# Kernel tuning notes

Hardware: AMD Instinct MI355X
Metric: run time of the kernel (lower is better)

The kernel has to match this reference:

```python
import jax, jax.numpy as jnp
import numpy as np
from jax import lax

HIDDEN = 256      # hidden_dim
LATENT = 128      # latent_dim
VOCAB = 32000     # vocab_size
MAX_LEN = 64      # max_len (stack capacity guard, as in original)
MAX_STEPS = 128   # fixed step budget for the decode stack machine
N_NODES = 511     # complete binary tree, depth 9


def _linear_params(key, fan_in, fan_out):
    k1, k2 = jax.random.split(key)
    s = 1.0 / np.sqrt(fan_in)
    W = jax.random.uniform(k1, (fan_out, fan_in), minval=-s, maxval=s, dtype=jnp.float32)
    b = jax.random.uniform(k2, (fan_out,), minval=-s, maxval=s, dtype=jnp.float32)
    return W, b


def setup_inputs() -> dict:
    key = jax.random.key(0)
    ks = jax.random.split(key, 10)
    embed = jax.random.normal(ks[0], (VOCAB, HIDDEN), dtype=jnp.float32)
    Wpar, bpar = _linear_params(ks[1], 3 * HIDDEN, HIDDEN)
    Wmu, bmu = _linear_params(ks[2], HIDDEN, LATENT)
    Wlv, blv = _linear_params(ks[3], HIDDEN, LATENT)
    W1, b1 = _linear_params(ks[4], LATENT, HIDDEN)
    W2, b2 = _linear_params(ks[5], HIDDEN, HIDDEN + 1)
    Wl, bl = _linear_params(ks[6], HIDDEN, VOCAB)
    Wp, bp = _linear_params(ks[7], HIDDEN, 2 * LATENT + VOCAB)
    values = jax.random.randint(ks[8], (N_NODES,), 0, VOCAB)
    idx = np.arange(N_NODES)
    left = np.where(2 * idx + 1 < N_NODES, 2 * idx + 1, -1).astype(np.int32)
    right = np.where(2 * idx + 2 < N_NODES, 2 * idx + 2, -1).astype(np.int32)
    eps = jax.random.normal(ks[9], (LATENT,), dtype=jnp.float32)
    return dict(embed=embed, Wpar=Wpar, bpar=bpar, Wmu=Wmu, bmu=bmu,
                Wlv=Wlv, blv=blv, W1=W1, b1=b1, W2=W2, b2=b2,
                Wl=Wl, bl=bl, Wp=Wp, bp=bp, eps=eps,
                values=jnp.asarray(values), left=jnp.asarray(left), right=jnp.asarray(right))


def reference(embed, Wpar, bpar, Wmu, bmu, Wlv, blv, W1, b1, W2, b2,
              Wl, bl, Wp, bp, eps, values, left, right):
    # ---------- encode: bottom-up over tree stored as index arrays ----------
    emb = embed[values]  # [N, H], one gather for all node embeddings

    def enc_step(h, i):
        v = emb[i]
        li = jnp.maximum(left[i], 0)
        ri = jnp.maximum(right[i], 0)
        cat = jnp.concatenate([v, h[li], h[ri]])          # [3H]
        hp = cat @ Wpar.T + bpar                           # parent combine
        hi = jnp.where(left[i] < 0, v, hp)                 # leaf -> embedding
        return h.at[i].set(hi), None

    h0 = jnp.zeros((values.shape[0], HIDDEN), dtype=embed.dtype)
    # children have larger index than parents -> process in descending order
    h, _ = lax.scan(enc_step, h0, jnp.arange(values.shape[0] - 1, -1, -1))
    root = h[0]
    mu = root @ Wmu.T + bmu
    logvar = root @ Wlv.T + blv
    z = mu + eps * jnp.exp(0.5 * logvar)                   # reparameterize

    # ---------- decode: stack machine with fixed step budget ----------
    V, L = VOCAB, LATENT
    stack0 = jnp.zeros((MAX_LEN, L), dtype=z.dtype).at[0].set(z)
    out0 = jnp.zeros((MAX_STEPS, V), dtype=z.dtype)

    def dec_step(state, _):
        stack, sp, out, op = state
        active = sp > 0
        idx = jnp.maximum(sp - 1, 0)
        node = stack[idx]                                  # pop
        hmid = jax.nn.leaky_relu(node @ W1.T + b1, 0.2)
        co = hmid @ W2.T + b2                              # [H+1]; co[0] = gate
        is_parent = (co[0] > 0) & (sp - 1 <= MAX_LEN - 2) & active

        def parent_fn(_):
            dec = co[1:] @ Wp.T + bp                       # [V + 2L]
            value = dec[:V]
            ll = dec[V:V + L]
            rl = dec[V + L:]
            # original appends llatent then rlatent -> rlatent on top
            st = stack.at[idx].set(ll).at[idx + 1].set(rl)
            return value, st, sp + 1

        def leaf_fn(_):
            return co[1:] @ Wl.T + bl, stack, sp - 1

        value, st, nsp = lax.cond(is_parent, parent_fn, leaf_fn, None)
        m = active.astype(z.dtype)
        out = out.at[op].add(m * value)                    # rows written once
        stack = jnp.where(active, st, stack)
        sp = jnp.where(active, nsp, sp)
        op = op + active.astype(op.dtype)
        return (stack, sp, out, op), None

    init = (stack0, jnp.int32(1), out0, jnp.int32(0))
    (_, _, out, _), _ = lax.scan(dec_step, init, None, length=MAX_STEPS)
    return out, mu, logvar
```

## Files before the change

kernel.cpp:

```cpp
#include <hip/hip_runtime.h>

#define HID 256
#define LAT 128
#define VOC 32000
#define NSTEP 128

__global__ __launch_bounds__(512)
void prep_kernel(const float* __restrict__ Wp, const float* __restrict__ W2,
                 const float* __restrict__ b2, const float* __restrict__ bp,
                 const float* __restrict__ Wpar,
                 const float* __restrict__ Wmu, const float* __restrict__ Wlv,
                 float* __restrict__ Wcomb, float* __restrict__ bcomb,
                 float* __restrict__ Wq_par, float* __restrict__ Wq_mu,
                 float* __restrict__ Wq_lv, float* __restrict__ Wq_w2) {
    const int b = blockIdx.x;
    const int t = threadIdx.x;
    if (b < 256) {
        const int o = b;
        const int k = t & 255, jh = t >> 8;
        __shared__ float wpt_s[256];
        __shared__ float part_s[2][256];
        __shared__ float red_s[4];
        if (t < 256) wpt_s[t] = Wp[(size_t)(VOC + o) * HID + t];
        __syncthreads();
        float acc = 0.f;
#pragma unroll 8
        for (int j = 0; j < 128; j++)
            acc += wpt_s[jh * 128 + j] * W2[(size_t)(1 + jh * 128 + j) * HID + k];
        part_s[jh][k] = acc;
        if (t < 256) {
            float p = wpt_s[k] * b2[1 + k];
            p += __shfl_xor(p, 1);  p += __shfl_xor(p, 2);  p += __shfl_xor(p, 4);
            p += __shfl_xor(p, 8);  p += __shfl_xor(p, 16); p += __shfl_xor(p, 32);
            if ((k & 63) == 0) red_s[k >> 6] = p;
        }
        __syncthreads();
        if (t < 256) Wcomb[(size_t)o * HID + k] = part_s[0][k] + part_s[1][k];
        if (t == 0) bcomb[o] = bp[VOC + o] + red_s[0] + red_s[1] + red_s[2] + red_s[3];
    } else if (b < 352) {
        const int k4 = (b - 256) * 2 + (t >> 8);
        const int r = t & 255;
        ((float4*)Wq_par)[k4 * 256 + r] = *(const float4*)(Wpar + (size_t)r * 768 + 4 * k4);
    } else if (b < 384) {
        const int k4 = (b - 352) * 2 + (t >> 8);
        const int r = t & 127, sel = (t >> 7) & 1;
        const float* src = (sel ? Wlv : Wmu) + (size_t)r * HID + 4 * k4;
        ((float4*)(sel ? Wq_lv : Wq_mu))[k4 * 128 + r] = *(const float4*)src;
    } else {
        const int k4 = (b - 384) * 2 + (t >> 8);
        const int r = t & 255;
        ((float4*)Wq_w2)[k4 * 256 + r] = *(const float4*)(W2 + (size_t)(1 + r) * HID + 4 * k4);
    }
}

__global__ __launch_bounds__(1024)
void enc2(const float* __restrict__ embed, const int* __restrict__ values,
          const float* __restrict__ Wq, const float* __restrict__ bpar,
          float* __restrict__ h, int base) {
    const int i = base + blockIdx.x;
    const int t = threadIdx.x;
    const int o = t & 255;
    const int g = t >> 8;
    const int cid = g & 1, kh = g >> 1;
    __shared__ __align__(16) float cat[2][768];
    __shared__ float part[4][256];
    __shared__ __align__(16) float pcat[768];

    const int c0n = 2 * i + 1;
    for (int q = t; q < 1536; q += 1024) {
        const int cc = (q >= 768);
        const int e = q - cc * 768;
        const int node = c0n + cc;
        const int seg = e >> 8, idx = e & 255;
        float v;
        if (seg == 0) v = embed[(size_t)values[node] * HID + idx];
        else {
            const int ch = 2 * node + seg;
            v = (ch >= 255) ? embed[(size_t)values[ch] * HID + idx]
                            : h[(size_t)ch * HID + idx];
        }
        cat[cc][e] = v;
    }
    __syncthreads();
    {
        const float4* wq = (const float4*)Wq + o;
        const float4* c4 = (const float4*)cat[cid] + kh * 96;
        float s0 = 0.f, s1 = 0.f, s2 = 0.f, s3 = 0.f;
#pragma unroll 8
        for (int k4 = 0; k4 < 96; k4 += 4) {
            const float4 wa = wq[(size_t)(kh * 96 + k4) * 256];
            const float4 wb = wq[(size_t)(kh * 96 + k4 + 1) * 256];
            const float4 wc = wq[(size_t)(kh * 96 + k4 + 2) * 256];
            const float4 wd = wq[(size_t)(kh * 96 + k4 + 3) * 256];
            const float4 ca = c4[k4], cb = c4[k4 + 1], cx = c4[k4 + 2], cd = c4[k4 + 3];
            s0 = fmaf(wa.x, ca.x, s0); s0 = fmaf(wa.y, ca.y, s0);
            s0 = fmaf(wa.z, ca.z, s0); s0 = fmaf(wa.w, ca.w, s0);
            s1 = fmaf(wb.x, cb.x, s1); s1 = fmaf(wb.y, cb.y, s1);
            s1 = fmaf(wb.z, cb.z, s1); s1 = fmaf(wb.w, cb.w, s1);
            s2 = fmaf(wc.x, cx.x, s2); s2 = fmaf(wc.y, cx.y, s2);
            s2 = fmaf(wc.z, cx.z, s2); s2 = fmaf(wc.w, cx.w, s2);
            s3 = fmaf(wd.x, cd.x, s3); s3 = fmaf(wd.y, cd.y, s3);
            s3 = fmaf(wd.z, cd.z, s3); s3 = fmaf(wd.w, cd.w, s3);
        }
        part[g][o] = (s0 + s1) + (s2 + s3);
    }
    __syncthreads();
    if (t < 512) {
        const int c = t >> 8;
        pcat[256 + (c << 8) + o] = part[c][o] + part[c + 2][o] + bpar[o];
    } else if (t < 768) {
        const int idx = t & 255;
        pcat[idx] = embed[(size_t)values[i] * HID + idx];
    }
    __syncthreads();
    {
        const float4* wq = (const float4*)Wq + o;
        const float4* c4 = (const float4*)pcat + g * 48;
        float s0 = 0.f, s1 = 0.f, s2 = 0.f, s3 = 0.f;
#pragma unroll
        for (int k4 = 0; k4 < 48; k4 += 4) {
            const float4 wa = wq[(size_t)(g * 48 + k4) * 256];
            const float4 wb = wq[(size_t)(g * 48 + k4 + 1) * 256];
            const float4 wc = wq[(size_t)(g * 48 + k4 + 2) * 256];
            const float4 wd = wq[(size_t)(g * 48 + k4 + 3) * 256];
            const float4 ca = c4[k4], cb = c4[k4 + 1], cx = c4[k4 + 2], cd = c4[k4 + 3];
            s0 = fmaf(wa.x, ca.x, s0); s0 = fmaf(wa.y, ca.y, s0);
            s0 = fmaf(wa.z, ca.z, s0); s0 = fmaf(wa.w, ca.w, s0);
            s1 = fmaf(wb.x, cb.x, s1); s1 = fmaf(wb.y, cb.y, s1);
            s1 = fmaf(wb.z, cb.z, s1); s1 = fmaf(wb.w, cb.w, s1);
            s2 = fmaf(wc.x, cx.x, s2); s2 = fmaf(wc.y, cx.y, s2);
            s2 = fmaf(wc.z, cx.z, s2); s2 = fmaf(wc.w, cx.w, s2);
            s3 = fmaf(wd.x, cd.x, s3); s3 = fmaf(wd.y, cd.y, s3);
            s3 = fmaf(wd.z, cd.z, s3); s3 = fmaf(wd.w, cd.w, s3);
        }
        part[g][o] = (s0 + s1) + (s2 + s3);
    }
    __syncthreads();
    if (t < 256)
        h[(size_t)i * HID + t] = part[0][t] + part[1][t] + part[2][t] + part[3][t] + bpar[t];
}

__global__ __launch_bounds__(1024)
void enc_final(const float* __restrict__ embed, const int* __restrict__ values,
               const float* __restrict__ Wq, const float* __restrict__ bpar,
               const float* __restrict__ h,
               const float* __restrict__ Wq_mu, const float* __restrict__ bmu,
               const float* __restrict__ Wq_lv, const float* __restrict__ blv,
               const float* __restrict__ eps,
               float* __restrict__ out, float* __restrict__ z) {
    const int t = threadIdx.x;
    const int o = t & 255;
    const int g = t >> 8;
    const int cid = g & 1, kh = g >> 1;
    __shared__ __align__(16) float cat[2][768];
    __shared__ float part[4][256];
    __shared__ __align__(16) float pcat[768];
    __shared__ __align__(16) float r0[256];
    __shared__ float mu_s[128], lv_s[128];

    for (int q = t; q < 1536; q += 1024) {
        const int cc = (q >= 768);
        const int e = q - cc * 768;
        const int node = 1 + cc;
        const int seg = e >> 8, idx = e & 255;
        cat[cc][e] = (seg == 0) ? embed[(size_t)values[node] * HID + idx]
                                : h[(size_t)(2 * node + seg) * HID + idx];
    }
    __syncthreads();
    {
        const float4* wq = (const float4*)Wq + o;
        const float4* c4 = (const float4*)cat[cid] + kh * 96;
        float s0 = 0.f, s1 = 0.f, s2 = 0.f, s3 = 0.f;
#pragma unroll 8
        for (int k4 = 0; k4 < 96; k4 += 4) {
            const float4 wa = wq[(size_t)(kh * 96 + k4) * 256];
            const float4 wb = wq[(size_t)(kh * 96 + k4 + 1) * 256];
            const float4 wc = wq[(size_t)(kh * 96 + k4 + 2) * 256];
            const float4 wd = wq[(size_t)(kh * 96 + k4 + 3) * 256];
            const float4 ca = c4[k4], cb = c4[k4 + 1], cx = c4[k4 + 2], cd = c4[k4 + 3];
            s0 = fmaf(wa.x, ca.x, s0); s0 = fmaf(wa.y, ca.y, s0);
            s0 = fmaf(wa.z, ca.z, s0); s0 = fmaf(wa.w, ca.w, s0);
            s1 = fmaf(wb.x, cb.x, s1); s1 = fmaf(wb.y, cb.y, s1);
            s1 = fmaf(wb.z, cb.z, s1); s1 = fmaf(wb.w, cb.w, s1);
            s2 = fmaf(wc.x, cx.x, s2); s2 = fmaf(wc.y, cx.y, s2);
            s2 = fmaf(wc.z, cx.z, s2); s2 = fmaf(wc.w, cx.w, s2);
            s3 = fmaf(wd.x, cd.x, s3); s3 = fmaf(wd.y, cd.y, s3);
            s3 = fmaf(wd.z, cd.z, s3); s3 = fmaf(wd.w, cd.w, s3);
        }
        part[g][o] = (s0 + s1) + (s2 + s3);
    }
    __syncthreads();
    if (t < 512) {
        const int c = t >> 8;
        pcat[256 + (c << 8) + o] = part[c][o] + part[c + 2][o] + bpar[o];
    } else if (t < 768) {
        const int idx = t & 255;
        pcat[idx] = embed[(size_t)values[0] * HID + idx];
    }
    __syncthreads();
    {
        const float4* wq = (const float4*)Wq + o;
        const float4* c4 = (const float4*)pcat + g * 48;
        float s0 = 0.f, s1 = 0.f, s2 = 0.f, s3 = 0.f;
#pragma unroll
        for (int k4 = 0; k4 < 48; k4 += 4) {
            const float4 wa = wq[(size_t)(g * 48 + k4) * 256];
            const float4 wb = wq[(size_t)(g * 48 + k4 + 1) * 256];
            const float4 wc = wq[(size_t)(g * 48 + k4 + 2) * 256];
            const float4 wd = wq[(size_t)(g * 48 + k4 + 3) * 256];
            const float4 ca = c4[k4], cb = c4[k4 + 1], cx = c4[k4 + 2], cd = c4[k4 + 3];
            s0 = fmaf(wa.x, ca.x, s0); s0 = fmaf(wa.y, ca.y, s0);
            s0 = fmaf(wa.z, ca.z, s0); s0 = fmaf(wa.w, ca.w, s0);
            s1 = fmaf(wb.x, cb.x, s1); s1 = fmaf(wb.y, cb.y, s1);
            s1 = fmaf(wb.z, cb.z, s1); s1 = fmaf(wb.w, cb.w, s1);
            s2 = fmaf(wc.x, cx.x, s2); s2 = fmaf(wc.y, cx.y, s2);
            s2 = fmaf(wc.z, cx.z, s2); s2 = fmaf(wc.w, cx.w, s2);
            s3 = fmaf(wd.x, cd.x, s3); s3 = fmaf(wd.y, cd.y, s3);
            s3 = fmaf(wd.z, cd.z, s3); s3 = fmaf(wd.w, cd.w, s3);
        }
        part[g][o] = (s0 + s1) + (s2 + s3);
    }
    __syncthreads();
    if (t < 256)
        r0[t] = part[0][t] + part[1][t] + part[2][t] + part[3][t] + bpar[t];
    __syncthreads();
    {
        const int r = o & 127;
        const float4* wqh = (const float4*)(o < 128 ? Wq_mu : Wq_lv) + r;
        const float4* r4 = (const float4*)r0 + g * 16;
        float s0 = 0.f, s1 = 0.f;
#pragma unroll
        for (int k4 = 0; k4 < 16; k4 += 2) {
            const float4 wa = wqh[(size_t)(g * 16 + k4) * 128];
            const float4 wb = wqh[(size_t)(g * 16 + k4 + 1) * 128];
            const float4 ca = r4[k4], cb = r4[k4 + 1];
            s0 = fmaf(wa.x, ca.x, s0); s0 = fmaf(wa.y, ca.y, s0);
            s0 = fmaf(wa.z, ca.z, s0); s0 = fmaf(wa.w, ca.w, s0);
            s1 = fmaf(wb.x, cb.x, s1); s1 = fmaf(wb.y, cb.y, s1);
            s1 = fmaf(wb.z, cb.z, s1); s1 = fmaf(wb.w, cb.w, s1);
        }
        part[g][o] = s0 + s1;
    }
    __syncthreads();
    if (t < 256) {
        const int r = t & 127;
        float v = part[0][t] + part[1][t] + part[2][t] + part[3][t];
        if (t < 128) { v += bmu[r]; out[(size_t)NSTEP * VOC + r] = v;       mu_s[r] = v; }
        else         { v += blv[r]; out[(size_t)NSTEP * VOC + 128 + r] = v; lv_s[r] = v; }
    }
    __syncthreads();
    if (t < 128) z[t] = mu_s[t] + eps[t] * expf(0.5f * lv_s[t]);
}

__global__ __launch_bounds__(512, 2)
void recur_kernel(const float* W1, const float* b1,
                  const float* W2, const float* b2,
                  const float* Wcomb, const float* bcomb,
                  const float* z,
                  float* Hrec, int* rowflag) {
    const int t = threadIdx.x;
    const int o = t >> 1;
    const int hk = t & 1;
    __shared__ __align__(16) float stack_s[64 * 128];
    __shared__ __align__(16) float hmid_s[256];

    float4 w1r[16];
#pragma unroll
    for (int j = 0; j < 16; j++)
        w1r[j] = *(const float4*)(W1 + (size_t)o * 128 + hk * 64 + 4 * j);
    float4 wcr[32];
#pragma unroll
    for (int j = 0; j < 32; j++)
        wcr[j] = *(const float4*)(Wcomb + (size_t)o * 256 + hk * 128 + 4 * j);

    const float b1o = b1[o];
    const float bco = bcomb[o];
    const float b20 = b2[0];
    const int l64 = t & 63;
    const float4 w2q = *(const float4*)(W2 + 4 * l64);

    if (t < 128) stack_s[t] = z[t];
    int sp = 1, op = 0;
    unsigned long long pm0 = 0ULL, pm1 = 0ULL;
    __syncthreads();

    for (int step = 0; step < NSTEP; step++) {
        if (sp <= 0) break;
        const int idx = sp - 1;

        const float* np = stack_s + idx * 128 + hk * 64;
        float a0 = 0.f, a1 = 0.f;
#pragma unroll
        for (int j = 0; j < 16; j += 2) {
            const float4 v0 = *(const float4*)(np + 4 * j);
            const float4 v1 = *(const float4*)(np + 4 * j + 4);
            a0 = fmaf(w1r[j].x, v0.x, a0);     a0 = fmaf(w1r[j].y, v0.y, a0);
            a0 = fmaf(w1r[j].z, v0.z, a0);     a0 = fmaf(w1r[j].w, v0.w, a0);
            a1 = fmaf(w1r[j + 1].x, v1.x, a1); a1 = fmaf(w1r[j + 1].y, v1.y, a1);
            a1 = fmaf(w1r[j + 1].z, v1.z, a1); a1 = fmaf(w1r[j + 1].w, v1.w, a1);
        }
        float a = a0 + a1;
        a += __shfl_xor(a, 1);
        if (hk == 0) {
            float pre = a + b1o;
            pre = pre > 0.f ? pre : 0.2f * pre;
            hmid_s[o] = pre;
            Hrec[(size_t)op * HID + o] = pre;
        }
        __syncthreads();

        const float4 hq = *(const float4*)(hmid_s + 4 * l64);
        float c = w2q.x * hq.x + w2q.y * hq.y + w2q.z * hq.z + w2q.w * hq.w;
        c += __shfl_xor(c, 1);  c += __shfl_xor(c, 2);  c += __shfl_xor(c, 4);
        c += __shfl_xor(c, 8);  c += __shfl_xor(c, 16); c += __shfl_xor(c, 32);
        const bool par = ((c + b20) > 0.f) && (sp <= 63);

        if (par) {
            const float* hp = hmid_s + hk * 128;
            float s0 = 0.f, s1 = 0.f, s2 = 0.f, s3 = 0.f;
#pragma unroll
            for (int j = 0; j < 32; j += 4) {
                const float4 v0 = *(const float4*)(hp + 4 * j);
                const float4 v1 = *(const float4*)(hp + 4 * j + 4);
                const float4 v2 = *(const float4*)(hp + 4 * j + 8);
                const float4 v3 = *(const float4*)(hp + 4 * j + 12);
                s0 = fmaf(wcr[j].x, v0.x, s0);     s0 = fmaf(wcr[j].y, v0.y, s0);
                s0 = fmaf(wcr[j].z, v0.z, s0);     s0 = fmaf(wcr[j].w, v0.w, s0);
                s1 = fmaf(wcr[j + 1].x, v1.x, s1); s1 = fmaf(wcr[j + 1].y, v1.y, s1);
                s1 = fmaf(wcr[j + 1].z, v1.z, s1); s1 = fmaf(wcr[j + 1].w, v1.w, s1);
                s2 = fmaf(wcr[j + 2].x, v2.x, s2); s2 = fmaf(wcr[j + 2].y, v2.y, s2);
                s2 = fmaf(wcr[j + 2].z, v2.z, s2); s2 = fmaf(wcr[j + 2].w, v2.w, s2);
                s3 = fmaf(wcr[j + 3].x, v3.x, s3); s3 = fmaf(wcr[j + 3].y, v3.y, s3);
                s3 = fmaf(wcr[j + 3].z, v3.z, s3); s3 = fmaf(wcr[j + 3].w, v3.w, s3);
            }
            float s = (s0 + s1) + (s2 + s3);
            s += __shfl_xor(s, 1);
            if (hk == 0)
                stack_s[(idx + (o >> 7)) * 128 + (o & 127)] = s + bco;
            if (op < 64) pm0 |= (1ULL << op); else pm1 |= (1ULL << (op - 64));
            sp += 1;
        } else {
            sp -= 1;
        }
        op++;
        __syncthreads();
    }

    if (t < 128) {
        int f = -1;
        if (t < op) f = (t < 64) ? (int)((pm0 >> t) & 1) : (int)((pm1 >> (t - 64)) & 1);
        rowflag[t] = f;
    }
}

__global__ __launch_bounds__(256)
void co1_kernel(const float* __restrict__ Hrec, const float* __restrict__ Wq_w2,
                const float* __restrict__ b2, const int* __restrict__ rowflag,
                float* __restrict__ Co1, int* __restrict__ lists) {
    const int r = blockIdx.x;
    const int c = threadIdx.x;
    if (r == 128) {
        if (c == 0) {
            int nl = 0, np_ = 0, nz = 0;
            for (int q = 0; q < 128; q++) {
                const int f = rowflag[q];
                if (f == 0) lists[nl++] = q;
                else if (f == 1) lists[128 + np_++] = q;
                else lists[256 + nz++] = q;
            }
            lists[384] = nl; lists[385] = np_; lists[386] = nz;
        }
        return;
    }
    __shared__ __align__(16) float hs[256];
    hs[c] = Hrec[(size_t)r * HID + c];
    __syncthreads();
    const float4* wq = (const float4*)Wq_w2 + c;
    const float4* h4 = (const float4*)hs;
    float s0 = b2[1 + c], s1 = 0.f, s2 = 0.f, s3 = 0.f;
#pragma unroll 8
    for (int k4 = 0; k4 < 64; k4 += 4) {
        const float4 a0 = wq[(k4) * 256],     h0 = h4[k4];
        const float4 a1 = wq[(k4 + 1) * 256], h1 = h4[k4 + 1];
        const float4 a2 = wq[(k4 + 2) * 256], h2 = h4[k4 + 2];
        const float4 a3 = wq[(k4 + 3) * 256], h3 = h4[k4 + 3];
        s0 = fmaf(a0.x, h0.x, s0); s0 = fmaf(a0.y, h0.y, s0);
        s0 = fmaf(a0.z, h0.z, s0); s0 = fmaf(a0.w, h0.w, s0);
        s1 = fmaf(a1.x, h1.x, s1); s1 = fmaf(a1.y, h1.y, s1);
        s1 = fmaf(a1.z, h1.z, s1); s1 = fmaf(a1.w, h1.w, s1);
        s2 = fmaf(a2.x, h2.x, s2); s2 = fmaf(a2.y, h2.y, s2);
        s2 = fmaf(a2.z, h2.z, s2); s2 = fmaf(a2.w, h2.w, s2);
        s3 = fmaf(a3.x, h3.x, s3); s3 = fmaf(a3.y, h3.y, s3);
        s3 = fmaf(a3.z, h3.z, s3); s3 = fmaf(a3.w, h3.w, s3);
    }
    Co1[(size_t)r * HID + c] = (s0 + s1) + (s2 + s3);
}

__global__ __launch_bounds__(256, 2)
void value_kernel(const float* __restrict__ Co1, const int* __restrict__ lists,
                  const float* __restrict__ Wl, const float* __restrict__ bl,
                  const float* __restrict__ Wp, const float* __restrict__ bp,
                  float* __restrict__ out) {
    const int m = blockIdx.y;
    const int t = threadIdx.x;
    const int v = blockIdx.x * 128 + (t & 127);
    const int rh = t >> 7;
    const int n = lists[384 + m];
    const int* list = lists + m * 128;
    const float* Wx = m ? Wp : Wl;
    const float* bx = m ? bp : bl;
    const float bv = bx[v];
    const float4* w4 = (const float4*)(Wx + (size_t)v * HID);

    for (int rc = 0; rc < n; rc += 32) {
        const int nr = min(32, n - rc);
        float acc[16];
#pragma unroll
        for (int i = 0; i < 16; i++) acc[i] = 0.f;
        for (int kc = 0; kc < 4; kc++) {
            float4 w[16];
#pragma unroll
            for (int i = 0; i < 16; i++) w[i] = w4[kc * 16 + i];
#pragma unroll
            for (int aa = 0; aa < 16; aa++) {
                const int rr = 2 * aa + rh;
                if (rr < nr) {
                    const int row = __builtin_amdgcn_readfirstlane(list[rc + rr]);
                    const float* cp = Co1 + (size_t)row * HID + kc * 64;
                    float s0 = 0.f, s1 = 0.f, s2 = 0.f, s3 = 0.f;
#pragma unroll
                    for (int i = 0; i < 16; i += 4) {
                        const float4 c0 = *(const float4*)(cp + 4 * i);
                        const float4 c1 = *(const float4*)(cp + 4 * i + 4);
                        const float4 c2 = *(const float4*)(cp + 4 * i + 8);
                        const float4 c3 = *(const float4*)(cp + 4 * i + 12);
                        s0 = fmaf(w[i].x, c0.x, s0);     s0 = fmaf(w[i].y, c0.y, s0);
                        s0 = fmaf(w[i].z, c0.z, s0);     s0 = fmaf(w[i].w, c0.w, s0);
                        s1 = fmaf(w[i + 1].x, c1.x, s1); s1 = fmaf(w[i + 1].y, c1.y, s1);
                        s1 = fmaf(w[i + 1].z, c1.z, s1); s1 = fmaf(w[i + 1].w, c1.w, s1);
                        s2 = fmaf(w[i + 2].x, c2.x, s2); s2 = fmaf(w[i + 2].y, c2.y, s2);
                        s2 = fmaf(w[i + 2].z, c2.z, s2); s2 = fmaf(w[i + 2].w, c2.w, s2);
                        s3 = fmaf(w[i + 3].x, c3.x, s3); s3 = fmaf(w[i + 3].y, c3.y, s3);
                        s3 = fmaf(w[i + 3].z, c3.z, s3); s3 = fmaf(w[i + 3].w, c3.w, s3);
                    }
                    acc[aa] += (s0 + s1) + (s2 + s3);
                }
            }
        }
#pragma unroll
        for (int aa = 0; aa < 16; aa++) {
            const int rr = 2 * aa + rh;
            if (rr < nr) {
                const int row = __builtin_amdgcn_readfirstlane(list[rc + rr]);
                out[(size_t)row * VOC + v] = acc[aa] + bv;
            }
        }
    }
    if (m == 0 && rh == 0) {
        const int nz = lists[386];
        const int* zl = lists + 256;
        for (int i = 0; i < nz; i++)
            out[(size_t)zl[i] * VOC + v] = 0.f;
    }
}

extern "C" void kernel_launch(void* const* d_in, const int* in_sizes, int n_in,
                              void* d_out, int out_size, void* d_ws, size_t ws_size,
                              hipStream_t stream) {
    const float* embed = (const float*)d_in[0];
    const float* Wpar  = (const float*)d_in[1];
    const float* bpar  = (const float*)d_in[2];
    const float* Wmu   = (const float*)d_in[3];
    const float* bmu   = (const float*)d_in[4];
    const float* Wlv   = (const float*)d_in[5];
    const float* blv   = (const float*)d_in[6];
    const float* W1    = (const float*)d_in[7];
    const float* b1    = (const float*)d_in[8];
    const float* W2    = (const float*)d_in[9];
    const float* b2    = (const float*)d_in[10];
    const float* Wl    = (const float*)d_in[11];
    const float* bl    = (const float*)d_in[12];
    const float* Wp    = (const float*)d_in[13];
    const float* bp    = (const float*)d_in[14];
    const float* eps   = (const float*)d_in[15];
    const int*  values = (const int*)d_in[16];

    float* ws = (float*)d_ws;
    float* h       = ws;
    float* z       = ws + 65280;
    float* Wcomb   = ws + 65408;
    float* bcomb   = ws + 130944;
    float* Hrec    = ws + 131200;
    float* Co1     = ws + 163968;
    int*   rowflag = (int*)(ws + 196736);
    float* Wq_par  = ws + 196864;
    float* Wq_mu   = ws + 393472;
    float* Wq_lv   = ws + 426240;
    float* Wq_w2   = ws + 459008;
    int*   lists   = (int*)(ws + 524544);
    float* out = (float*)d_out;

    prep_kernel<<<416, 512, 0, stream>>>(Wp, W2, b2, bp, Wpar, Wmu, Wlv,
                                         Wcomb, bcomb, Wq_par, Wq_mu, Wq_lv, Wq_w2);

    enc2<<<64, 1024, 0, stream>>>(embed, values, Wq_par, bpar, h, 63);
    enc2<<<16, 1024, 0, stream>>>(embed, values, Wq_par, bpar, h, 15);
    enc2<<< 4, 1024, 0, stream>>>(embed, values, Wq_par, bpar, h,  3);
    enc_final<<<1, 1024, 0, stream>>>(embed, values, Wq_par, bpar, h,
                                      Wq_mu, bmu, Wq_lv, blv, eps, out, z);

    recur_kernel<<<1, 512, 0, stream>>>(W1, b1, W2, b2, Wcomb, bcomb, z, Hrec, rowflag);

    co1_kernel<<<129, 256, 0, stream>>>(Hrec, Wq_w2, b2, rowflag, Co1, lists);
    value_kernel<<<dim3(250, 2), 256, 0, stream>>>(Co1, lists, Wl, bl, Wp, bp, out);
}
```

Baseline: 277.7 us.

## Split upper encoder levels across many blocks and hoist stack projection before gate

The top encoder levels, previously handled by a few blocks or a single block, now run in a new per-level kernel. It splits each node's 256 outputs into column slices across 64 blocks, and a small head kernel computes mu, logvar and z. This spreads the weight-streaming work of the near-serial tree levels over many compute units, at the cost of more kernel launches. In the recurrent decode loop, the child-latent projection is now computed before the gate reduction instead of only on parent steps. This removes the branch dependency so the two reductions can overlap, but it does redundant work on leaf steps.

```diff
diff --git a/kernel.cpp b/kernel.cpp
--- a/kernel.cpp
+++ b/kernel.cpp
@@ -140,114 +140,84 @@
         h[(size_t)i * HID + t] = part[0][t] + part[1][t] + part[2][t] + part[3][t] + bpar[t];
 }
 
-__global__ __launch_bounds__(1024)
-void enc_final(const float* __restrict__ embed, const int* __restrict__ values,
-               const float* __restrict__ Wq, const float* __restrict__ bpar,
-               const float* __restrict__ h,
-               const float* __restrict__ Wq_mu, const float* __restrict__ bmu,
-               const float* __restrict__ Wq_lv, const float* __restrict__ blv,
-               const float* __restrict__ eps,
-               float* __restrict__ out, float* __restrict__ z) {
-    const int t = threadIdx.x;
-    const int o = t & 255;
-    const int g = t >> 8;
-    const int cid = g & 1, kh = g >> 1;
-    __shared__ __align__(16) float cat[2][768];
-    __shared__ float part[4][256];
-    __shared__ __align__(16) float pcat[768];
+__global__ __launch_bounds__(256)
+void enc_lvl(const float* __restrict__ embed, const int* __restrict__ values,
+             const float* __restrict__ Wq, const float* __restrict__ bpar,
+             float* __restrict__ h, int first, int logS) {
+    const int S = 1 << logS;
+    const int R = 256 >> logS;
+    const int node = first + (blockIdx.x >> logS);
+    const int slice = blockIdx.x & (S - 1);
+    const int t = threadIdx.x;
+    const int rl = t & (R - 1);
+    const int g = t >> (8 - logS);
+    __shared__ __align__(16) float cat_s[768];
+    __shared__ float part_s[256];
+
+    for (int e = t; e < 768; e += 256) {
+        const int seg = e >> 8, idx = e & 255;
+        cat_s[e] = (seg == 0) ? embed[(size_t)values[node] * HID + idx]
+                              : h[(size_t)(2 * node + seg) * HID + idx];
+    }
+    __syncthreads();
+
+    const int r0 = slice * R;
+    const int nk4 = 192 >> logS;
+    const float4* wq = (const float4*)Wq + (size_t)(g * nk4) * 256 + r0 + rl;
+    const float4* c4 = (const float4*)cat_s + g * nk4;
+    float s0 = 0.f, s1 = 0.f, s2 = 0.f, s3 = 0.f;
+    for (int k4 = 0; k4 < nk4; k4 += 4) {
+        const float4 wa = wq[(size_t)(k4) * 256];
+        const float4 wb = wq[(size_t)(k4 + 1) * 256];
+        const float4 wc = wq[(size_t)(k4 + 2) * 256];
+        const float4 wd = wq[(size_t)(k4 + 3) * 256];
+        const float4 ca = c4[k4], cb = c4[k4 + 1], cx = c4[k4 + 2], cd = c4[k4 + 3];
+        s0 = fmaf(wa.x, ca.x, s0); s0 = fmaf(wa.y, ca.y, s0);
+        s0 = fmaf(wa.z, ca.z, s0); s0 = fmaf(wa.w, ca.w, s0);
+        s1 = fmaf(wb.x, cb.x, s1); s1 = fmaf(wb.y, cb.y, s1);
+        s1 = fmaf(wb.z, cb.z, s1); s1 = fmaf(wb.w, cb.w, s1);
+        s2 = fmaf(wc.x, cx.x, s2); s2 = fmaf(wc.y, cx.y, s2);
+        s2 = fmaf(wc.z, cx.z, s2); s2 = fmaf(wc.w, cx.w, s2);
+        s3 = fmaf(wd.x, cd.x, s3); s3 = fmaf(wd.y, cd.y, s3);
+        s3 = fmaf(wd.z, cd.z, s3); s3 = fmaf(wd.w, cd.w, s3);
+    }
+    part_s[t] = (s0 + s1) + (s2 + s3);
+    __syncthreads();
+    if (t < R) {
+        float v = bpar[r0 + t];
+        for (int g2 = 0; g2 < S; g2++) v += part_s[g2 * R + t];
+        h[(size_t)node * HID + r0 + t] = v;
+    }
+}
+
+__global__ __launch_bounds__(256)
+void head_kernel(const float* __restrict__ h,
+                 const float* __restrict__ Wq_mu, const float* __restrict__ bmu,
+                 const float* __restrict__ Wq_lv, const float* __restrict__ blv,
+                 const float* __restrict__ eps,
+                 float* __restrict__ out, float* __restrict__ z) {
+    const int t = threadIdx.x;
     __shared__ __align__(16) float r0[256];
     __shared__ float mu_s[128], lv_s[128];
-
-    for (int q = t; q < 1536; q += 1024) {
-        const int cc = (q >= 768);
-        const int e = q - cc * 768;
-        const int node = 1 + cc;
-        const int seg = e >> 8, idx = e & 255;
-        cat[cc][e] = (seg == 0) ? embed[(size_t)values[node] * HID + idx]
-                                : h[(size_t)(2 * node + seg) * HID + idx];
-    }
-    __syncthreads();
-    {
-        const float4* wq = (const float4*)Wq + o;
-        const float4* c4 = (const float4*)cat[cid] + kh * 96;
-        float s0 = 0.f, s1 = 0.f, s2 = 0.f, s3 = 0.f;
-#pragma unroll 8
-        for (int k4 = 0; k4 < 96; k4 += 4) {
-            const float4 wa = wq[(size_t)(kh * 96 + k4) * 256];
-            const float4 wb = wq[(size_t)(kh * 96 + k4 + 1) * 256];
-            const float4 wc = wq[(size_t)(kh * 96 + k4 + 2) * 256];
-            const float4 wd = wq[(size_t)(kh * 96 + k4 + 3) * 256];
-            const float4 ca = c4[k4], cb = c4[k4 + 1], cx = c4[k4 + 2], cd = c4[k4 + 3];
-            s0 = fmaf(wa.x, ca.x, s0); s0 = fmaf(wa.y, ca.y, s0);
-            s0 = fmaf(wa.z, ca.z, s0); s0 = fmaf(wa.w, ca.w, s0);
-            s1 = fmaf(wb.x, cb.x, s1); s1 = fmaf(wb.y, cb.y, s1);
-            s1 = fmaf(wb.z, cb.z, s1); s1 = fmaf(wb.w, cb.w, s1);
-            s2 = fmaf(wc.x, cx.x, s2); s2 = fmaf(wc.y, cx.y, s2);
-            s2 = fmaf(wc.z, cx.z, s2); s2 = fmaf(wc.w, cx.w, s2);
-            s3 = fmaf(wd.x, cd.x, s3); s3 = fmaf(wd.y, cd.y, s3);
-            s3 = fmaf(wd.z, cd.z, s3); s3 = fmaf(wd.w, cd.w, s3);
-        }
-        part[g][o] = (s0 + s1) + (s2 + s3);
-    }
-    __syncthreads();
-    if (t < 512) {
-        const int c = t >> 8;
-        pcat[256 + (c << 8) + o] = part[c][o] + part[c + 2][o] + bpar[o];
-    } else if (t < 768) {
-        const int idx = t & 255;
-        pcat[idx] = embed[(size_t)values[0] * HID + idx];
-    }
-    __syncthreads();
-    {
-        const float4* wq = (const float4*)Wq + o;
-        const float4* c4 = (const float4*)pcat + g * 48;
-        float s0 = 0.f, s1 = 0.f, s2 = 0.f, s3 = 0.f;
-#pragma unroll
-        for (int k4 = 0; k4 < 48; k4 += 4) {
-            const float4 wa = wq[(size_t)(g * 48 + k4) * 256];
-            const float4 wb = wq[(size_t)(g * 48 + k4 + 1) * 256];
-            const float4 wc = wq[(size_t)(g * 48 + k4 + 2) * 256];
-            const float4 wd = wq[(size_t)(g * 48 + k4 + 3) * 256];
-            const float4 ca = c4[k4], cb = c4[k4 + 1], cx = c4[k4 + 2], cd = c4[k4 + 3];
-            s0 = fmaf(wa.x, ca.x, s0); s0 = fmaf(wa.y, ca.y, s0);
-            s0 = fmaf(wa.z, ca.z, s0); s0 = fmaf(wa.w, ca.w, s0);
-            s1 = fmaf(wb.x, cb.x, s1); s1 = fmaf(wb.y, cb.y, s1);
-            s1 = fmaf(wb.z, cb.z, s1); s1 = fmaf(wb.w, cb.w, s1);
-            s2 = fmaf(wc.x, cx.x, s2); s2 = fmaf(wc.y, cx.y, s2);
-            s2 = fmaf(wc.z, cx.z, s2); s2 = fmaf(wc.w, cx.w, s2);
-            s3 = fmaf(wd.x, cd.x, s3); s3 = fmaf(wd.y, cd.y, s3);
-            s3 = fmaf(wd.z, cd.z, s3); s3 = fmaf(wd.w, cd.w, s3);
-        }
-        part[g][o] = (s0 + s1) + (s2 + s3);
-    }
-    __syncthreads();
-    if (t < 256)
-        r0[t] = part[0][t] + part[1][t] + part[2][t] + part[3][t] + bpar[t];
-    __syncthreads();
-    {
-        const int r = o & 127;
-        const float4* wqh = (const float4*)(o < 128 ? Wq_mu : Wq_lv) + r;
-        const float4* r4 = (const float4*)r0 + g * 16;
-        float s0 = 0.f, s1 = 0.f;
-#pragma unroll
-        for (int k4 = 0; k4 < 16; k4 += 2) {
-            const float4 wa = wqh[(size_t)(g * 16 + k4) * 128];
-            const float4 wb = wqh[(size_t)(g * 16 + k4 + 1) * 128];
-            const float4 ca = r4[k4], cb = r4[k4 + 1];
-            s0 = fmaf(wa.x, ca.x, s0); s0 = fmaf(wa.y, ca.y, s0);
-            s0 = fmaf(wa.z, ca.z, s0); s0 = fmaf(wa.w, ca.w, s0);
-            s1 = fmaf(wb.x, cb.x, s1); s1 = fmaf(wb.y, cb.y, s1);
-            s1 = fmaf(wb.z, cb.z, s1); s1 = fmaf(wb.w, cb.w, s1);
-        }
-        part[g][o] = s0 + s1;
-    }
-    __syncthreads();
-    if (t < 256) {
-        const int r = t & 127;
-        float v = part[0][t] + part[1][t] + part[2][t] + part[3][t];
-        if (t < 128) { v += bmu[r]; out[(size_t)NSTEP * VOC + r] = v;       mu_s[r] = v; }
-        else         { v += blv[r]; out[(size_t)NSTEP * VOC + 128 + r] = v; lv_s[r] = v; }
-    }
+    r0[t] = h[t];
+    __syncthreads();
+    const int r = t & 127;
+    const float4* wqh = (const float4*)(t < 128 ? Wq_mu : Wq_lv) + r;
+    const float4* r4 = (const float4*)r0;
+    float s0 = 0.f, s1 = 0.f;
+#pragma unroll
+    for (int k4 = 0; k4 < 64; k4 += 2) {
+        const float4 wa = wqh[(size_t)k4 * 128];
+        const float4 wb = wqh[(size_t)(k4 + 1) * 128];
+        const float4 ca = r4[k4], cb = r4[k4 + 1];
+        s0 = fmaf(wa.x, ca.x, s0); s0 = fmaf(wa.y, ca.y, s0);
+        s0 = fmaf(wa.z, ca.z, s0); s0 = fmaf(wa.w, ca.w, s0);
+        s1 = fmaf(wb.x, cb.x, s1); s1 = fmaf(wb.y, cb.y, s1);
+        s1 = fmaf(wb.z, cb.z, s1); s1 = fmaf(wb.w, cb.w, s1);
+    }
+    float v = s0 + s1 + (t < 128 ? bmu[r] : blv[r]);
+    out[(size_t)NSTEP * VOC + t] = v;
+    if (t < 128) mu_s[r] = v; else lv_s[r] = v;
     __syncthreads();
     if (t < 128) z[t] = mu_s[t] + eps[t] * expf(0.5f * lv_s[t]);
 }
@@ -311,30 +281,32 @@
 
         const float4 hq = *(const float4*)(hmid_s + 4 * l64);
         float c = w2q.x * hq.x + w2q.y * hq.y + w2q.z * hq.z + w2q.w * hq.w;
+
+        const float* hp = hmid_s + hk * 128;
+        float s0 = 0.f, s1 = 0.f, s2 = 0.f, s3 = 0.f;
+#pragma unroll
+        for (int j = 0; j < 32; j += 4) {
+            const float4 v0 = *(const float4*)(hp + 4 * j);
+            const float4 v1 = *(const float4*)(hp + 4 * j + 4);
+            const float4 v2 = *(const float4*)(hp + 4 * j + 8);
+            const float4 v3 = *(const float4*)(hp + 4 * j + 12);
+            s0 = fmaf(wcr[j].x, v0.x, s0);     s0 = fmaf(wcr[j].y, v0.y, s0);
+            s0 = fmaf(wcr[j].z, v0.z, s0);     s0 = fmaf(wcr[j].w, v0.w, s0);
+            s1 = fmaf(wcr[j + 1].x, v1.x, s1); s1 = fmaf(wcr[j + 1].y, v1.y, s1);
+            s1 = fmaf(wcr[j + 1].z, v1.z, s1); s1 = fmaf(wcr[j + 1].w, v1.w, s1);
+            s2 = fmaf(wcr[j + 2].x, v2.x, s2); s2 = fmaf(wcr[j + 2].y, v2.y, s2);
+            s2 = fmaf(wcr[j + 2].z, v2.z, s2); s2 = fmaf(wcr[j + 2].w, v2.w, s2);
+            s3 = fmaf(wcr[j + 3].x, v3.x, s3); s3 = fmaf(wcr[j + 3].y, v3.y, s3);
+            s3 = fmaf(wcr[j + 3].z, v3.z, s3); s3 = fmaf(wcr[j + 3].w, v3.w, s3);
+        }
+        float s = (s0 + s1) + (s2 + s3);
+        s += __shfl_xor(s, 1);
+
         c += __shfl_xor(c, 1);  c += __shfl_xor(c, 2);  c += __shfl_xor(c, 4);
         c += __shfl_xor(c, 8);  c += __shfl_xor(c, 16); c += __shfl_xor(c, 32);
         const bool par = ((c + b20) > 0.f) && (sp <= 63);
 
         if (par) {
-            const float* hp = hmid_s + hk * 128;
-            float s0 = 0.f, s1 = 0.f, s2 = 0.f, s3 = 0.f;
-#pragma unroll
-            for (int j = 0; j < 32; j += 4) {
-                const float4 v0 = *(const float4*)(hp + 4 * j);
-                const float4 v1 = *(const float4*)(hp + 4 * j + 4);
-                const float4 v2 = *(const float4*)(hp + 4 * j + 8);
-                const float4 v3 = *(const float4*)(hp + 4 * j + 12);
-                s0 = fmaf(wcr[j].x, v0.x, s0);     s0 = fmaf(wcr[j].y, v0.y, s0);
-                s0 = fmaf(wcr[j].z, v0.z, s0);     s0 = fmaf(wcr[j].w, v0.w, s0);
-                s1 = fmaf(wcr[j + 1].x, v1.x, s1); s1 = fmaf(wcr[j + 1].y, v1.y, s1);
-                s1 = fmaf(wcr[j + 1].z, v1.z, s1); s1 = fmaf(wcr[j + 1].w, v1.w, s1);
-                s2 = fmaf(wcr[j + 2].x, v2.x, s2); s2 = fmaf(wcr[j + 2].y, v2.y, s2);
-                s2 = fmaf(wcr[j + 2].z, v2.z, s2); s2 = fmaf(wcr[j + 2].w, v2.w, s2);
-                s3 = fmaf(wcr[j + 3].x, v3.x, s3); s3 = fmaf(wcr[j + 3].y, v3.y, s3);
-                s3 = fmaf(wcr[j + 3].z, v3.z, s3); s3 = fmaf(wcr[j + 3].w, v3.w, s3);
-            }
-            float s = (s0 + s1) + (s2 + s3);
-            s += __shfl_xor(s, 1);
             if (hk == 0)
                 stack_s[(idx + (o >> 7)) * 128 + (o & 127)] = s + bco;
             if (op < 64) pm0 |= (1ULL << op); else pm1 |= (1ULL << (op - 64));
@@ -504,10 +476,13 @@
                                          Wcomb, bcomb, Wq_par, Wq_mu, Wq_lv, Wq_w2);
 
     enc2<<<64, 1024, 0, stream>>>(embed, values, Wq_par, bpar, h, 63);
-    enc2<<<16, 1024, 0, stream>>>(embed, values, Wq_par, bpar, h, 15);
-    enc2<<< 4, 1024, 0, stream>>>(embed, values, Wq_par, bpar, h,  3);
-    enc_final<<<1, 1024, 0, stream>>>(embed, values, Wq_par, bpar, h,
-                                      Wq_mu, bmu, Wq_lv, blv, eps, out, z);
+    enc_lvl<<<64, 256, 0, stream>>>(embed, values, Wq_par, bpar, h, 31, 1);
+    enc_lvl<<<64, 256, 0, stream>>>(embed, values, Wq_par, bpar, h, 15, 2);
+    enc_lvl<<<64, 256, 0, stream>>>(embed, values, Wq_par, bpar, h,  7, 3);
+    enc_lvl<<<64, 256, 0, stream>>>(embed, values, Wq_par, bpar, h,  3, 4);
+    enc_lvl<<<32, 256, 0, stream>>>(embed, values, Wq_par, bpar, h,  1, 4);
+    enc_lvl<<<16, 256, 0, stream>>>(embed, values, Wq_par, bpar, h,  0, 4);
+    head_kernel<<<1, 256, 0, stream>>>(h, Wq_mu, bmu, Wq_lv, blv, eps, out, z);
 
     recur_kernel<<<1, 512, 0, stream>>>(W1, b1, W2, b2, Wcomb, bcomb, z, Hrec, rowflag);
 
```

Measured after the change: 245.6 us. 11.6% less time.
